# Optimization experiments

Hardware: AMD Instinct MI355X
Metric: run time of the kernel (lower is better)

The kernel has to match this reference:

```python
import jax, jax.numpy as jnp
import numpy as np

N = 302       # connectome neurons
T = 2048      # R * window_size
K = 33        # inference-network temporal kernel (valid conv)
TE = T + K - 1  # extended time length before cropping
ODOR = 16
DT = 0.2


def _dwconv(x, w):
    """Per-neuron valid temporal conv. x: (N, Te), w: (N, K) -> (N, Te-K+1)."""
    return jax.lax.conv_general_dilated(
        x[None], w[:, None, :], window_strides=(1,), padding='VALID',
        feature_group_count=x.shape[0],
        dimension_numbers=('NCH', 'OIH', 'NCH'))[0]


def setup_inputs() -> dict:
    key = jax.random.key(0)
    ks = jax.random.split(key, 24)
    u = lambda k, s: jax.random.uniform(k, s, dtype=jnp.float32)
    g = lambda k, s: jax.random.normal(k, s, dtype=jnp.float32)
    inp = {}
    # forward tensor args
    inp['fluorescence_raw_target'] = u(ks[0], (N, TE))
    inp['fluorescence_full_target'] = u(ks[1], (N, T))
    inp['odor_input'] = u(ks[2], (ODOR, TE))
    inp['eps'] = g(ks[3], (N, T))  # reparameterization noise
    # encoder (Linear odor -> per-neuron sensory drive)
    inp['W_enc'] = g(ks[4], (N, ODOR)) * 0.1
    inp['b_enc'] = jnp.zeros((N,), jnp.float32)
    inp['sensory_mask'] = (u(ks[5], (N,)) < 0.15).astype(jnp.float32)
    # inference network (per-neuron depthwise temporal convs -> mu, logvar)
    inp['W_mu_f'] = g(ks[6], (N, K)) * 0.1
    inp['W_mu_s'] = g(ks[7], (N, K)) * 0.1
    inp['b_mu'] = g(ks[8], (N,)) * 0.01
    inp['W_lv_f'] = g(ks[9], (N, K)) * 0.1
    inp['W_lv_s'] = g(ks[10], (N, K)) * 0.1
    inp['b_lv'] = -2.0 + g(ks[11], (N,)) * 0.01
    # connectome-constrained recurrent weights (sparsity*signs*magnitudes folded in)
    inp['W_chem'] = (u(ks[12], (N, N)) < 0.05).astype(jnp.float32) * g(ks[13], (N, N)) * 0.1
    inp['W_elec'] = (u(ks[14], (N, N)) < 0.05).astype(jnp.float32) * g(ks[15], (N, N)) * 0.1
    inp['bias'] = g(ks[16], (N,)) * 0.1
    inp['tau'] = 0.1 + u(ks[17], (N,))
    # voltage -> calcium activation (NeuronWiseAffine)
    inp['w_aff'] = 0.5 + u(ks[18], (N,))
    inp['b_aff'] = g(ks[19], (N,)) * 0.1
    # calcium -> fluorescence (NeuronWiseLinear)
    inp['scale'] = 0.5 + u(ks[20], (N,))
    inp['shift'] = g(ks[21], (N,)) * 0.1
    # calcium decay time constant
    inp['calcium_tau'] = 0.5 + 1.5 * u(ks[22], (N,))
    return inp


def reference(fluorescence_raw_target, fluorescence_full_target, odor_input, eps,
              W_enc, b_enc, sensory_mask,
              W_mu_f, W_mu_s, b_mu, W_lv_f, W_lv_s, b_lv,
              W_chem, W_elec, bias, tau,
              w_aff, b_aff, scale, shift, calcium_tau):
    # --- encoder: sensory drive masked to sensory neurons, (N, TE) ---
    sensory_input_extend = sensory_mask[:, None] * (W_enc @ odor_input + b_enc[:, None])
    # --- inference network q(V | F, S): valid depthwise temporal convs ---
    mu_v = _dwconv(fluorescence_raw_target, W_mu_f) + _dwconv(sensory_input_extend, W_mu_s) + b_mu[:, None]
    logvar_v = _dwconv(fluorescence_raw_target, W_lv_f) + _dwconv(sensory_input_extend, W_lv_s) + b_lv[:, None]
    sample_v = mu_v + jnp.exp(0.5 * logvar_v) * eps  # (N, T)
    Tlat = mu_v.shape[1]
    crop = (sensory_input_extend.shape[1] - Tlat) // 2
    sensory_input = sensory_input_extend[:, crop:sensory_input_extend.shape[1] - crop]  # (N, T)
    # --- network dynamics: one-step leaky-integrator prediction ---
    act = jax.nn.relu(sample_v)
    recurrent_in = W_chem @ act + W_elec @ sample_v + sensory_input
    mu_neuron_voltage_prob = sample_v + (DT / tau)[:, None] * (-sample_v + recurrent_in + bias[:, None])
    # --- voltage -> calcium activation (NeuronWiseAffine, softplus) ---
    calcium_activation = jax.nn.softplus(w_aff[:, None] * sample_v + b_aff[:, None])
    # --- SCF exponential: causal exp(-t*alpha) filter + initial-calcium decay ---
    init_calcium = (fluorescence_full_target[:, 0] - shift) / scale  # (N,)
    alpha = DT / calcium_tau                               # (N,)
    t = jnp.arange(Tlat, dtype=jnp.float32)
    kern = jnp.exp(-t * alpha[:, None])                    # (N, T)
    conv = jax.vmap(lambda xn, kn: jnp.convolve(xn, kn)[:Tlat])(calcium_activation, kern)
    mu_calcium = conv + init_calcium[:, None] * kern       # (N, T)
    mu_calcium_prob = mu_calcium[None]                     # (1, N, T)
    # --- calcium -> fluorescence (NeuronWiseLinear) ---
    mu_fluorescence_trace_prob = scale[:, None] * mu_calcium + shift[:, None]
    return (mu_neuron_voltage_prob, mu_fluorescence_trace_prob, mu_v, logvar_v,
            sample_v, calcium_activation, mu_calcium_prob, recurrent_in, sensory_input)
```

## Files before the change

### kernel.cpp

```cpp
#include <hip/hip_runtime.h>
#include <hip/hip_bf16.h>

#define Nn 302
#define Tt 2048
#define TEx 2080
#define Kk 33
#define ODOR 16
#define DTc 0.2f
#define NT (Nn*Tt)
#define NKB 20
#define NMT 19
#define NNT 128

typedef __attribute__((ext_vector_type(8))) short short8;
typedef __attribute__((ext_vector_type(4))) float f32x4;

__device__ __forceinline__ unsigned short f2bu(float x){ __hip_bfloat16 h = __float2bfloat16(x); unsigned short u; __builtin_memcpy(&u, &h, 2); return u; }

__device__ __forceinline__ void ld8(const float* p, size_t i, float* v){
    float4 a = *(const float4*)(p + i);
    float4 b = *(const float4*)(p + i + 4);
    v[0]=a.x; v[1]=a.y; v[2]=a.z; v[3]=a.w;
    v[4]=b.x; v[5]=b.y; v[6]=b.z; v[7]=b.w;
}
__device__ __forceinline__ void st8(float* p, size_t i, const float* v){
    *(float4*)(p + i)     = make_float4(v[0],v[1],v[2],v[3]);
    *(float4*)(p + i + 4) = make_float4(v[4],v[5],v[6],v[7]);
}

__device__ __forceinline__ float* region(void* outv, int r){
    return (float*)outv + (size_t)r * NT;
}

__global__ __launch_bounds__(256) void kA(
    const float* __restrict__ fr, const float* __restrict__ odor,
    const float* __restrict__ eps,
    const float* __restrict__ Wenc, const float* __restrict__ benc,
    const float* __restrict__ mask,
    const float* __restrict__ Wmf, const float* __restrict__ Wms,
    const float* __restrict__ bmu,
    const float* __restrict__ Wlf, const float* __restrict__ Wls,
    const float* __restrict__ blv,
    const float* __restrict__ waff, const float* __restrict__ baff,
    const float* __restrict__ fft, const float* __restrict__ scal,
    const float* __restrict__ shft, const float* __restrict__ ctau,
    void* outv)
{
    __shared__ float frs[TEx];
    __shared__ float ses[TEx];
    __shared__ float Bsc[256];
    __shared__ float Psc[256];
    __shared__ float wv[4*Kk + ODOR];

    const int n = blockIdx.x;
    const int tid = threadIdx.x;
    float* wmf_s = wv;        float* wms_s = wv + Kk;
    float* wlf_s = wv + 2*Kk; float* wls_s = wv + 3*Kk;
    float* wenc_s = wv + 4*Kk;

    if (tid < Kk){
        wmf_s[tid] = Wmf[n*Kk+tid];
        wms_s[tid] = Wms[n*Kk+tid];
        wlf_s[tid] = Wlf[n*Kk+tid];
        wls_s[tid] = Wls[n*Kk+tid];
    }
    if (tid < ODOR) wenc_s[tid] = Wenc[n*ODOR+tid];

    for (int c = tid; c < TEx/8; c += 256){
        float v[8];
        ld8(fr, (size_t)n*TEx + c*8, v);
        #pragma unroll
        for (int j = 0; j < 8; j++) frs[c*8+j] = v[j];
    }
    __syncthreads();

    const float benc_f = benc[n];
    const float mask_f = mask[n];
    for (int c = tid; c < TEx/8; c += 256){
        float acc[8];
        #pragma unroll
        for (int j = 0; j < 8; j++) acc[j] = benc_f;
        #pragma unroll
        for (int o = 0; o < ODOR; o++){
            float v[8];
            ld8(odor, (size_t)o*TEx + c*8, v);
            #pragma unroll
            for (int j = 0; j < 8; j++) acc[j] = fmaf(wenc_s[o], v[j], acc[j]);
        }
        #pragma unroll
        for (int j = 0; j < 8; j++) ses[c*8+j] = mask_f*acc[j];
    }
    __syncthreads();

    const float bmu_f  = bmu[n];
    const float blv_f  = blv[n];
    const float waff_f = waff[n];
    const float baff_f = baff[n];

    const int t0 = tid*8;
    float xf[40], xs[40];
    #pragma unroll
    for (int i = 0; i < 10; i++){
        float4 a = *(const float4*)&frs[t0 + 4*i];
        xf[4*i]=a.x; xf[4*i+1]=a.y; xf[4*i+2]=a.z; xf[4*i+3]=a.w;
        float4 b = *(const float4*)&ses[t0 + 4*i];
        xs[4*i]=b.x; xs[4*i+1]=b.y; xs[4*i+2]=b.z; xs[4*i+3]=b.w;
    }

    float aMu[8], aLv[8];
    #pragma unroll
    for (int j = 0; j < 8; j++){ aMu[j]=bmu_f; aLv[j]=blv_f; }
    #pragma unroll
    for (int k = 0; k < Kk; k++){
        float wf=wmf_s[k], wsn=wms_s[k], vf=wlf_s[k], vsn=wls_s[k];
        #pragma unroll
        for (int j = 0; j < 8; j++){
            aMu[j] = fmaf(xf[j+k], wf, fmaf(xs[j+k], wsn, aMu[j]));
            aLv[j] = fmaf(xf[j+k], vf, fmaf(xs[j+k], vsn, aLv[j]));
        }
    }

    const size_t base = (size_t)n*Tt + t0;
    float ev[8];
    ld8(eps, base, ev);

    float smp[8], cav[8], siv[8];
    #pragma unroll
    for (int j = 0; j < 8; j++){
        float s = aMu[j] + expf(0.5f*aLv[j])*ev[j];
        smp[j] = s;
        float x = waff_f*s + baff_f;
        cav[j] = (x > 20.f) ? x : log1pf(expf(x));
        siv[j] = ses[t0 + j + 16];
    }

    st8(region(outv,2), base, aMu);
    st8(region(outv,3), base, aLv);
    st8(region(outv,4), base, smp);
    st8(region(outv,5), base, cav);
    st8(region(outv,8), base, siv);

    const float sc = scal[n];
    const float sh = shft[n];
    const float ct = ctau[n];
    const float decay = expf(-DTc/ct);

    float b = 0.f;
    #pragma unroll
    for (int j = 0; j < 8; j++) b = fmaf(decay, b, cav[j]);
    Bsc[tid] = b;
    __syncthreads();

    if (tid < 64){
        const float d2 = decay*decay, d4 = d2*d2, d8 = d4*d4;
        const float d16 = d8*d8, d32 = d16*d16;
        float g0=Bsc[4*tid], g1=Bsc[4*tid+1], g2=Bsc[4*tid+2], g3=Bsc[4*tid+3];
        float G = fmaf(d8, fmaf(d8, fmaf(d8, g0, g1), g2), g3);
        float S = G, pw = d32;
        #pragma unroll
        for (int off = 1; off < 64; off <<= 1){
            float up = __shfl_up(S, off, 64);
            if (tid >= off) S = fmaf(pw, up, S);
            pw = pw*pw;
        }
        float E = __shfl_up(S, 1, 64);
        if (tid == 0) E = 0.f;
        const float init = (fft[(size_t)n*Tt] - sh)/sc;
        float P = fmaf(init, __powf(d32, (float)tid), E);
        #pragma unroll
        for (int j = 0; j < 4; j++){ Psc[4*tid+j] = P; P = fmaf(d8, P, Bsc[4*tid+j]); }
    }
    __syncthreads();

    float c = Psc[tid];
    float mc[8], fl[8];
    #pragma unroll
    for (int j = 0; j < 8; j++){
        c = fmaf(decay, c, cav[j]);
        mc[j] = c;
        fl[j] = fmaf(sc, c, sh);
    }
    st8(region(outv,6), base, mc);
    st8(region(outv,1), base, fl);
}

__global__ __launch_bounds__(256) void kTP(
    const float* __restrict__ Wch, const float* __restrict__ Wel,
    void* outv, unsigned short* __restrict__ xt_sw, unsigned short* __restrict__ wc_sw)
{
    __shared__ unsigned short tile[64][68];
    const int blk = blockIdx.x;
    const int tid = threadIdx.x;

    if (blk >= 160){
        const int mt = blk - 160;
        for (int i = 0; i < 5; i++){
            const int fid = tid + 256*i;
            const int kb = fid >> 6, l = fid & 63;
            const int ln = l & 15, quad = l >> 4;
            const int m = mt*16 + ln;
            const int k0 = kb*32 + quad*8;
            unsigned short v[8];
            #pragma unroll
            for (int j = 0; j < 8; j++){
                const int k = k0 + j;
                float x = 0.f;
                if (m < Nn){
                    if (k < Nn)                      x = Wch[(size_t)m*Nn + k];
                    else if (k >= 320 && k < 320+Nn) x = Wel[(size_t)m*Nn + (k-320)];
                }
                v[j] = f2bu(x);
            }
            *(uint4*)(wc_sw + ((size_t)(mt*NKB + kb)*64 + l)*8) =
                make_uint4((unsigned)v[0]|((unsigned)v[1]<<16), (unsigned)v[2]|((unsigned)v[3]<<16),
                           (unsigned)v[4]|((unsigned)v[5]<<16), (unsigned)v[6]|((unsigned)v[7]<<16));
        }
        return;
    }

    const float* o_sv = region(outv, 4);
    const int bx = blk & 31;
    const int m0 = (blk >> 5) * 64;
    const int t0 = bx*64;
    const int c = tid & 7, r0 = tid >> 3;

    #pragma unroll
    for (int h = 0; h < 2; h++){
        const int r = r0 + 32*h;
        const int m = m0 + r;
        float v[8] = {0,0,0,0,0,0,0,0};
        if (m < Nn) ld8(o_sv, (size_t)m*Tt + t0 + c*8, v);
        unsigned short* d = &tile[r][c*8];
        #pragma unroll
        for (int j = 0; j < 8; j++) d[j] = f2bu(v[j]);
    }
    __syncthreads();

    const int kb0 = m0 >> 5;
    #pragma unroll
    for (int i = 0; i < 2; i++){
        const int fid = tid + 256*i;
        const int nt_loc = fid >> 7;
        const int kb_loc = (fid >> 6) & 1;
        const int l  = fid & 63;
        const int ln = l & 15, quad = l >> 4;
        const int nt = bx*4 + nt_loc;
        unsigned short sv[8], av[8];
        #pragma unroll
        for (int j = 0; j < 8; j++){
            unsigned short u = tile[kb_loc*32 + quad*8 + j][nt_loc*16 + ln];
            sv[j] = u;
            av[j] = (u & 0x8000u) ? (unsigned short)0 : u;
        }
        *(uint4*)(xt_sw + ((size_t)(nt*NKB + kb0 + kb_loc)*64 + l)*8) =
            make_uint4((unsigned)av[0]|((unsigned)av[1]<<16), (unsigned)av[2]|((unsigned)av[3]<<16),
                       (unsigned)av[4]|((unsigned)av[5]<<16), (unsigned)av[6]|((unsigned)av[7]<<16));
        *(uint4*)(xt_sw + ((size_t)(nt*NKB + 10 + kb0 + kb_loc)*64 + l)*8) =
            make_uint4((unsigned)sv[0]|((unsigned)sv[1]<<16), (unsigned)sv[2]|((unsigned)sv[3]<<16),
                       (unsigned)sv[4]|((unsigned)sv[5]<<16), (unsigned)sv[6]|((unsigned)sv[7]<<16));
    }
}

__global__ __launch_bounds__(256) void kG(
    const unsigned short* __restrict__ wc_sw, const unsigned short* __restrict__ xt_sw,
    const float* __restrict__ bias, const float* __restrict__ tau,
    void* outv)
{
    __shared__ float C[16][68];
    const int tid = threadIdx.x;
    const int wave = tid >> 6, lane = tid & 63;
    const int ln = lane & 15, quad = lane >> 4;
    const int bx = blockIdx.x, by = blockIdx.y;
    const int nt = bx*4 + wave;

    const unsigned short* Ap = wc_sw + (size_t)by*NKB*512 + lane*8;
    const unsigned short* Bp = xt_sw + (size_t)nt*NKB*512 + lane*8;

    f32x4 acc = {0.f,0.f,0.f,0.f};
    #pragma unroll
    for (int kb = 0; kb < NKB; kb++){
        short8 a = *(const short8*)(Ap + kb*512);
        short8 b = *(const short8*)(Bp + kb*512);
        acc = __builtin_amdgcn_mfma_f32_16x16x32_bf16(a, b, acc, 0, 0, 0);
    }

    #pragma unroll
    for (int r = 0; r < 4; r++) C[quad*4 + r][wave*16 + ln] = acc[r];
    __syncthreads();

    if (tid < 128){
        const int m_loc = tid >> 3, strip = tid & 7;
        const int m = by*16 + m_loc;
        if (m < Nn){
            const float* o_sv = region(outv, 4);
            const float* o_si = region(outv, 8);
            float* o_mnv = region(outv, 0);
            float* o_rec = region(outv, 7);
            const int t = bx*64 + strip*8;
            const size_t idx = (size_t)m*Tt + t;
            float si[8], sv[8], rec[8], mnv[8];
            ld8(o_si, idx, si);
            ld8(o_sv, idx, sv);
            const float it = DTc / tau[m];
            const float bi = bias[m];
            #pragma unroll
            for (int j = 0; j < 8; j++){
                float rc = C[m_loc][strip*8 + j] + si[j];
                rec[j] = rc;
                mnv[j] = sv[j] + it*(-sv[j] + rc + bi);
            }
            st8(o_rec, idx, rec);
            st8(o_mnv, idx, mnv);
        }
    }
}

__global__ __launch_bounds__(256) void kBs(
    const float* __restrict__ Wch, const float* __restrict__ Wel,
    const float* __restrict__ bias, const float* __restrict__ tau,
    void* outv)
{
    const int tx = threadIdx.x & 63, ty = threadIdx.x >> 6;
    const int t  = blockIdx.x*64 + tx;
    const int n0 = blockIdx.y*32;

    const float* o_sv = region(outv, 4);
    const float* o_si = region(outv, 8);
    float* o_mnv = region(outv, 0);
    float* o_rec = region(outv, 7);

    int nn[8]; size_t pb[8]; float acc[8];
    #pragma unroll
    for (int r = 0; r < 8; r++){
        int v = n0 + ty + 4*r;
        nn[r] = v;
        pb[r] = (size_t)((v < Nn) ? v : 0) * 151;
        acc[r] = 0.f;
    }
    for (int mh = 0; mh < 151; mh++){
        const int m = mh*2;
        float s0 = o_sv[(size_t)m*Tt + t];
        float s1 = o_sv[(size_t)(m+1)*Tt + t];
        float a0 = fmaxf(s0,0.f), a1 = fmaxf(s1,0.f);
        #pragma unroll
        for (int r = 0; r < 8; r++){
            float2 wc = ((const float2*)Wch)[pb[r] + mh];
            float2 we = ((const float2*)Wel)[pb[r] + mh];
            acc[r] = fmaf(wc.x, a0, acc[r]);
            acc[r] = fmaf(wc.y, a1, acc[r]);
            acc[r] = fmaf(we.x, s0, acc[r]);
            acc[r] = fmaf(we.y, s1, acc[r]);
        }
    }
    #pragma unroll
    for (int r = 0; r < 8; r++){
        if (nn[r] < Nn){
            const size_t idx = (size_t)nn[r]*Tt + t;
            float rec = acc[r] + o_si[idx];
            o_rec[idx] = rec;
            float sv = o_sv[idx];
            o_mnv[idx] = sv + (DTc/tau[nn[r]])*(-sv + rec + bias[nn[r]]);
        }
    }
}

extern "C" void kernel_launch(void* const* d_in, const int* in_sizes, int n_in,
                              void* d_out, int out_size, void* d_ws, size_t ws_size,
                              hipStream_t stream) {
    const float* fr   = (const float*)d_in[0];
    const float* fft  = (const float*)d_in[1];
    const float* odor = (const float*)d_in[2];
    const float* eps  = (const float*)d_in[3];
    const float* Wenc = (const float*)d_in[4];
    const float* benc = (const float*)d_in[5];
    const float* mask = (const float*)d_in[6];
    const float* Wmf  = (const float*)d_in[7];
    const float* Wms  = (const float*)d_in[8];
    const float* bmu  = (const float*)d_in[9];
    const float* Wlf  = (const float*)d_in[10];
    const float* Wls  = (const float*)d_in[11];
    const float* blv  = (const float*)d_in[12];
    const float* Wch  = (const float*)d_in[13];
    const float* Wel  = (const float*)d_in[14];
    const float* bias = (const float*)d_in[15];
    const float* tau  = (const float*)d_in[16];
    const float* waff = (const float*)d_in[17];
    const float* baff = (const float*)d_in[18];
    const float* scal = (const float*)d_in[19];
    const float* shft = (const float*)d_in[20];
    const float* ctau = (const float*)d_in[21];

    kA<<<Nn, 256, 0, stream>>>(fr, odor, eps, Wenc, benc, mask, Wmf, Wms, bmu,
                               Wlf, Wls, blv, waff, baff, fft, scal, shft, ctau, d_out);

    const size_t XT_ELEMS = (size_t)NNT*NKB*64*8;
    const size_t WS_NEED  = (XT_ELEMS + (size_t)NMT*NKB*64*8) * 2;
    if (ws_size >= WS_NEED){
        unsigned short* xt_sw = (unsigned short*)d_ws;
        unsigned short* wc_sw = xt_sw + XT_ELEMS;
        kTP<<<160 + NMT, 256, 0, stream>>>(Wch, Wel, d_out, xt_sw, wc_sw);
        kG<<<dim3(32, NMT), 256, 0, stream>>>(wc_sw, xt_sw, bias, tau, d_out);
    } else {
        kBs<<<dim3(32, 10), 256, 0, stream>>>(Wch, Wel, bias, tau, d_out);
    }
}
```

Measured before the change: 151.0 us.

## Fuse bf16 transpose/packing into MFMA recurrent GEMM kernel, drop workspace pass

Removes the separate kTP kernel that converted sample_v and the weights to swizzled bf16 tiles in workspace. The fused kGF kernel now packs the 16-row weight tile into shared memory per block and reads sample_v directly from global memory, converting to bf16 (with relu for the chemical path) in registers before two MFMA accumulations. This saves one kernel launch and a global round trip through workspace. In exchange every block re-reads and converts its weight slice, and the B operand comes from strided column loads of sample_v that are re-read across the 19 row blocks. The scalar fallback kernel is also removed.

```diff
diff --git a/kernel.cpp b/kernel.cpp
--- a/kernel.cpp
+++ b/kernel.cpp
@@ -8,9 +8,7 @@
 #define ODOR 16
 #define DTc 0.2f
 #define NT (Nn*Tt)
-#define NKB 20
 #define NMT 19
-#define NNT 128
 
 typedef __attribute__((ext_vector_type(8))) short short8;
 typedef __attribute__((ext_vector_type(4))) float f32x4;
@@ -184,120 +182,79 @@
     st8(region(outv,1), base, fl);
 }
 
-__global__ __launch_bounds__(256) void kTP(
+__global__ __launch_bounds__(256) void kGF(
     const float* __restrict__ Wch, const float* __restrict__ Wel,
-    void* outv, unsigned short* __restrict__ xt_sw, unsigned short* __restrict__ wc_sw)
-{
-    __shared__ unsigned short tile[64][68];
-    const int blk = blockIdx.x;
-    const int tid = threadIdx.x;
-
-    if (blk >= 160){
-        const int mt = blk - 160;
-        for (int i = 0; i < 5; i++){
-            const int fid = tid + 256*i;
-            const int kb = fid >> 6, l = fid & 63;
-            const int ln = l & 15, quad = l >> 4;
-            const int m = mt*16 + ln;
-            const int k0 = kb*32 + quad*8;
-            unsigned short v[8];
-            #pragma unroll
-            for (int j = 0; j < 8; j++){
-                const int k = k0 + j;
-                float x = 0.f;
-                if (m < Nn){
-                    if (k < Nn)                      x = Wch[(size_t)m*Nn + k];
-                    else if (k >= 320 && k < 320+Nn) x = Wel[(size_t)m*Nn + (k-320)];
-                }
-                v[j] = f2bu(x);
-            }
-            *(uint4*)(wc_sw + ((size_t)(mt*NKB + kb)*64 + l)*8) =
-                make_uint4((unsigned)v[0]|((unsigned)v[1]<<16), (unsigned)v[2]|((unsigned)v[3]<<16),
-                           (unsigned)v[4]|((unsigned)v[5]<<16), (unsigned)v[6]|((unsigned)v[7]<<16));
-        }
-        return;
-    }
-
-    const float* o_sv = region(outv, 4);
-    const int bx = blk & 31;
-    const int m0 = (blk >> 5) * 64;
-    const int t0 = bx*64;
-    const int c = tid & 7, r0 = tid >> 3;
-
-    #pragma unroll
-    for (int h = 0; h < 2; h++){
-        const int r = r0 + 32*h;
-        const int m = m0 + r;
-        float v[8] = {0,0,0,0,0,0,0,0};
-        if (m < Nn) ld8(o_sv, (size_t)m*Tt + t0 + c*8, v);
-        unsigned short* d = &tile[r][c*8];
-        #pragma unroll
-        for (int j = 0; j < 8; j++) d[j] = f2bu(v[j]);
-    }
-    __syncthreads();
-
-    const int kb0 = m0 >> 5;
-    #pragma unroll
-    for (int i = 0; i < 2; i++){
-        const int fid = tid + 256*i;
-        const int nt_loc = fid >> 7;
-        const int kb_loc = (fid >> 6) & 1;
-        const int l  = fid & 63;
-        const int ln = l & 15, quad = l >> 4;
-        const int nt = bx*4 + nt_loc;
-        unsigned short sv[8], av[8];
-        #pragma unroll
-        for (int j = 0; j < 8; j++){
-            unsigned short u = tile[kb_loc*32 + quad*8 + j][nt_loc*16 + ln];
-            sv[j] = u;
-            av[j] = (u & 0x8000u) ? (unsigned short)0 : u;
-        }
-        *(uint4*)(xt_sw + ((size_t)(nt*NKB + kb0 + kb_loc)*64 + l)*8) =
-            make_uint4((unsigned)av[0]|((unsigned)av[1]<<16), (unsigned)av[2]|((unsigned)av[3]<<16),
-                       (unsigned)av[4]|((unsigned)av[5]<<16), (unsigned)av[6]|((unsigned)av[7]<<16));
-        *(uint4*)(xt_sw + ((size_t)(nt*NKB + 10 + kb0 + kb_loc)*64 + l)*8) =
-            make_uint4((unsigned)sv[0]|((unsigned)sv[1]<<16), (unsigned)sv[2]|((unsigned)sv[3]<<16),
-                       (unsigned)sv[4]|((unsigned)sv[5]<<16), (unsigned)sv[6]|((unsigned)sv[7]<<16));
-    }
-}
-
-__global__ __launch_bounds__(256) void kG(
-    const unsigned short* __restrict__ wc_sw, const unsigned short* __restrict__ xt_sw,
     const float* __restrict__ bias, const float* __restrict__ tau,
     void* outv)
 {
+    __shared__ unsigned short As[20*64*8];
     __shared__ float C[16][68];
+
     const int tid = threadIdx.x;
     const int wave = tid >> 6, lane = tid & 63;
     const int ln = lane & 15, quad = lane >> 4;
     const int bx = blockIdx.x, by = blockIdx.y;
-    const int nt = bx*4 + wave;
-
-    const unsigned short* Ap = wc_sw + (size_t)by*NKB*512 + lane*8;
-    const unsigned short* Bp = xt_sw + (size_t)nt*NKB*512 + lane*8;
-
-    f32x4 acc = {0.f,0.f,0.f,0.f};
-    #pragma unroll
-    for (int kb = 0; kb < NKB; kb++){
-        short8 a = *(const short8*)(Ap + kb*512);
-        short8 b = *(const short8*)(Bp + kb*512);
-        acc = __builtin_amdgcn_mfma_f32_16x16x32_bf16(a, b, acc, 0, 0, 0);
-    }
-
-    #pragma unroll
-    for (int r = 0; r < 4; r++) C[quad*4 + r][wave*16 + ln] = acc[r];
+
+    for (int s = tid; s < 20*64; s += 256){
+        const int kbp = s >> 6, l = s & 63;
+        const int pass = kbp / 10, kb = kbp - pass*10;
+        const int lm = l & 15, lq = l >> 4;
+        const int m = by*16 + lm;
+        const int k0 = kb*32 + lq*8;
+        const float* W = pass ? Wel : Wch;
+        unsigned short v[8];
+        #pragma unroll
+        for (int j = 0; j < 8; j++){
+            const int k = k0 + j;
+            float x = (m < Nn && k < Nn) ? W[(size_t)m*Nn + k] : 0.f;
+            v[j] = f2bu(x);
+        }
+        *(uint4*)(As + (size_t)s*8) = make_uint4(
+            (unsigned)v[0]|((unsigned)v[1]<<16), (unsigned)v[2]|((unsigned)v[3]<<16),
+            (unsigned)v[4]|((unsigned)v[5]<<16), (unsigned)v[6]|((unsigned)v[7]<<16));
+    }
+    __syncthreads();
+
+    const float* o_sv = region(outv, 4);
+    const int t = (bx*4 + wave)*16 + ln;
+
+    f32x4 accC = {0.f,0.f,0.f,0.f};
+    f32x4 accE = {0.f,0.f,0.f,0.f};
+    #pragma unroll
+    for (int kb = 0; kb < 10; kb++){
+        const int k0 = kb*32 + quad*8;
+        short8 ac = *(const short8*)(As + ((size_t)( kb     *64 + lane))*8);
+        short8 ae = *(const short8*)(As + ((size_t)((10+kb)*64 + lane))*8);
+        float bv[8];
+        #pragma unroll
+        for (int j = 0; j < 8; j++){
+            int k = k0 + j;
+            if (k > Nn-1) k = Nn-1;
+            bv[j] = o_sv[(size_t)k*Tt + t];
+        }
+        short8 bc, be;
+        #pragma unroll
+        for (int j = 0; j < 8; j++){
+            be[j] = (short)f2bu(bv[j]);
+            bc[j] = (short)f2bu(fmaxf(bv[j], 0.f));
+        }
+        accC = __builtin_amdgcn_mfma_f32_16x16x32_bf16(ac, bc, accC, 0, 0, 0);
+        accE = __builtin_amdgcn_mfma_f32_16x16x32_bf16(ae, be, accE, 0, 0, 0);
+    }
+
+    #pragma unroll
+    for (int r = 0; r < 4; r++) C[quad*4 + r][wave*16 + ln] = accC[r] + accE[r];
     __syncthreads();
 
     if (tid < 128){
         const int m_loc = tid >> 3, strip = tid & 7;
         const int m = by*16 + m_loc;
         if (m < Nn){
-            const float* o_sv = region(outv, 4);
             const float* o_si = region(outv, 8);
             float* o_mnv = region(outv, 0);
             float* o_rec = region(outv, 7);
-            const int t = bx*64 + strip*8;
-            const size_t idx = (size_t)m*Tt + t;
+            const int tt = bx*64 + strip*8;
+            const size_t idx = (size_t)m*Tt + tt;
             float si[8], sv[8], rec[8], mnv[8];
             ld8(o_si, idx, si);
             ld8(o_sv, idx, sv);
@@ -311,55 +268,6 @@
             }
             st8(o_rec, idx, rec);
             st8(o_mnv, idx, mnv);
-        }
-    }
-}
-
-__global__ __launch_bounds__(256) void kBs(
-    const float* __restrict__ Wch, const float* __restrict__ Wel,
-    const float* __restrict__ bias, const float* __restrict__ tau,
-    void* outv)
-{
-    const int tx = threadIdx.x & 63, ty = threadIdx.x >> 6;
-    const int t  = blockIdx.x*64 + tx;
-    const int n0 = blockIdx.y*32;
-
-    const float* o_sv = region(outv, 4);
-    const float* o_si = region(outv, 8);
-    float* o_mnv = region(outv, 0);
-    float* o_rec = region(outv, 7);
-
-    int nn[8]; size_t pb[8]; float acc[8];
-    #pragma unroll
-    for (int r = 0; r < 8; r++){
-        int v = n0 + ty + 4*r;
-        nn[r] = v;
-        pb[r] = (size_t)((v < Nn) ? v : 0) * 151;
-        acc[r] = 0.f;
-    }
-    for (int mh = 0; mh < 151; mh++){
-        const int m = mh*2;
-        float s0 = o_sv[(size_t)m*Tt + t];
-        float s1 = o_sv[(size_t)(m+1)*Tt + t];
-        float a0 = fmaxf(s0,0.f), a1 = fmaxf(s1,0.f);
-        #pragma unroll
-        for (int r = 0; r < 8; r++){
-            float2 wc = ((const float2*)Wch)[pb[r] + mh];
-            float2 we = ((const float2*)Wel)[pb[r] + mh];
-            acc[r] = fmaf(wc.x, a0, acc[r]);
-            acc[r] = fmaf(wc.y, a1, acc[r]);
-            acc[r] = fmaf(we.x, s0, acc[r]);
-            acc[r] = fmaf(we.y, s1, acc[r]);
-        }
-    }
-    #pragma unroll
-    for (int r = 0; r < 8; r++){
-        if (nn[r] < Nn){
-            const size_t idx = (size_t)nn[r]*Tt + t;
-            float rec = acc[r] + o_si[idx];
-            o_rec[idx] = rec;
-            float sv = o_sv[idx];
-            o_mnv[idx] = sv + (DTc/tau[nn[r]])*(-sv + rec + bias[nn[r]]);
         }
     }
 }
@@ -390,17 +298,10 @@
     const float* shft = (const float*)d_in[20];
     const float* ctau = (const float*)d_in[21];
 
+    (void)d_ws; (void)ws_size;
+
     kA<<<Nn, 256, 0, stream>>>(fr, odor, eps, Wenc, benc, mask, Wmf, Wms, bmu,
                                Wlf, Wls, blv, waff, baff, fft, scal, shft, ctau, d_out);
 
-    const size_t XT_ELEMS = (size_t)NNT*NKB*64*8;
-    const size_t WS_NEED  = (XT_ELEMS + (size_t)NMT*NKB*64*8) * 2;
-    if (ws_size >= WS_NEED){
-        unsigned short* xt_sw = (unsigned short*)d_ws;
-        unsigned short* wc_sw = xt_sw + XT_ELEMS;
-        kTP<<<160 + NMT, 256, 0, stream>>>(Wch, Wel, d_out, xt_sw, wc_sw);
-        kG<<<dim3(32, NMT), 256, 0, stream>>>(wc_sw, xt_sw, bias, tau, d_out);
-    } else {
-        kBs<<<dim3(32, 10), 256, 0, stream>>>(Wch, Wel, bias, tau, d_out);
-    }
-}
+    kGF<<<dim3(32, NMT), 256, 0, stream>>>(Wch, Wel, bias, tau, d_out);
+}
```

After: 152.4 us. Within noise of the previous version (+1.0%).
